# Optimization experiments

Hardware: AMD Instinct MI355X
Metric: run time of the kernel (lower is better)

Reference implementation:

```python
import jax, jax.numpy as jnp
import numpy as np

POOL_H, POOL_W = 7, 7
SCALE = 0.25
SAMPLING = 2  # fixed sampling ratio (static grid)


def _sample_coords(lo, bin_sz, pool, s):
    # lo: [N], bin_sz: [N] -> coords [N, pool*s]
    # point iy within bin: (iy + 0.5) / s of a bin
    offs = (jnp.arange(pool)[:, None] + (jnp.arange(s)[None, :] + 0.5) / s).reshape(-1)  # [pool*s]
    return lo[:, None] + offs[None, :] * bin_sz[:, None]


def roi_align(feat, rois, roibatches):
    B, C, H, W = feat.shape
    N = rois.shape[0]
    x1 = rois[:, 0] * SCALE
    y1 = rois[:, 1] * SCALE
    x2 = rois[:, 2] * SCALE
    y2 = rois[:, 3] * SCALE
    roi_w = jnp.maximum(x2 - x1, 1.0)
    roi_h = jnp.maximum(y2 - y1, 1.0)
    bin_w = roi_w / POOL_W
    bin_h = roi_h / POOL_H

    ys = _sample_coords(y1, bin_h, POOL_H, SAMPLING)  # [N, Gy]
    xs = _sample_coords(x1, bin_w, POOL_W, SAMPLING)  # [N, Gx]
    Gy, Gx = ys.shape[1], xs.shape[1]

    vy = (ys >= -1.0) & (ys <= H)  # out-of-range samples contribute 0
    vx = (xs >= -1.0) & (xs <= W)

    yc = jnp.clip(ys, 0.0, H - 1)
    xc = jnp.clip(xs, 0.0, W - 1)
    y_lo = jnp.clip(jnp.floor(yc).astype(jnp.int32), 0, H - 1)
    x_lo = jnp.clip(jnp.floor(xc).astype(jnp.int32), 0, W - 1)
    y_hi = jnp.minimum(y_lo + 1, H - 1)
    x_hi = jnp.minimum(x_lo + 1, W - 1)
    ly = yc - y_lo  # [N, Gy]
    lx = xc - x_lo  # [N, Gx]
    hy = 1.0 - ly
    hx = 1.0 - lx

    b = roibatches.astype(jnp.int32)[:, None, None]  # [N,1,1]

    def gather(yi, xi):
        # advanced indexing -> [N, Gy, Gx, C]
        return feat[b, :, yi[:, :, None], xi[:, None, :]]

    v_ll = gather(y_lo, x_lo)
    v_lh = gather(y_lo, x_hi)
    v_hl = gather(y_hi, x_lo)
    v_hh = gather(y_hi, x_hi)

    wy_l = (hy * vy)[:, :, None, None]
    wy_h = (ly * vy)[:, :, None, None]
    wx_l = (hx * vx)[:, None, :, None]
    wx_h = (lx * vx)[:, None, :, None]

    vals = (wy_l * wx_l * v_ll + wy_l * wx_h * v_lh
            + wy_h * wx_l * v_hl + wy_h * wx_h * v_hh)  # [N, Gy, Gx, C]

    # average pool over the SAMPLING x SAMPLING points per bin
    vals = vals.reshape(N, POOL_H, SAMPLING, POOL_W, SAMPLING, C)
    out = vals.mean(axis=(2, 4))  # [N, POOL_H, POOL_W, C]
    return jnp.transpose(out, (0, 3, 1, 2))  # [N, C, POOL_H, POOL_W]


def setup_inputs() -> dict:
    key = jax.random.key(0)
    k1, k2, k3, k4 = jax.random.split(key, 4)
    B, C, H, W = 4, 256, 200, 304
    N = 1024
    img_h, img_w = H / SCALE, W / SCALE
    feat = jax.random.normal(k1, (B, C, H, W), dtype=jnp.float32)
    xa = jax.random.uniform(k2, (N, 2), minval=0.0, maxval=img_w)
    ya = jax.random.uniform(k3, (N, 2), minval=0.0, maxval=img_h)
    rois = jnp.stack([xa.min(1), ya.min(1), xa.max(1), ya.max(1)], axis=1).astype(jnp.float32)
    roibatches = jax.random.randint(k4, (N,), 0, B, dtype=jnp.int32)
    return {"feat": feat, "rois": rois, "roibatches": roibatches}


def reference(feat, rois, roibatches):
    return roi_align(feat, rois, roibatches)
```

## Files before the change

### kernel.cpp

```cpp
#include <hip/hip_runtime.h>
#include <hip/hip_bf16.h>


#define POOL 7
constexpr int Bc = 4;
constexpr int Cc = 256;
constexpr int Hc = 200;
constexpr int Wc = 304;
constexpr int HWc = Hc * Wc;
constexpr float SCALEc = 0.25f;
constexpr int STR = 129;

static __device__ __forceinline__ float bf16_lo(unsigned u) {
    u <<= 16;
    return __builtin_bit_cast(float, u);
}
static __device__ __forceinline__ float bf16_hi(unsigned u) {
    u &= 0xFFFF0000u;
    return __builtin_bit_cast(float, u);
}
static __device__ __forceinline__ unsigned pack_bf16(float f0, float f1) {
    unsigned u0 = (unsigned)__hip_bfloat16_raw(__float2bfloat16(f0)).x;
    unsigned u1 = (unsigned)__hip_bfloat16_raw(__float2bfloat16(f1)).x;
    return u0 | (u1 << 16);
}

__global__ __launch_bounds__(1024) void sort_rois_by_batch(
    const int* __restrict__ rb, int* __restrict__ perm, int N)
{
    __shared__ int wave_cnt[16][4];
    __shared__ int bucket_base[4];
    int t    = threadIdx.x;
    int w    = t >> 6;
    int lane = t & 63;
    int b    = (t < N) ? rb[t] : -1;

    unsigned long long m[4];
#pragma unroll
    for (int k = 0; k < 4; ++k) m[k] = __ballot(b == k);
    if (lane == 0) {
#pragma unroll
        for (int k = 0; k < 4; ++k) wave_cnt[w][k] = __popcll(m[k]);
    }
    __syncthreads();
    if (t == 0) {
        int base = 0;
#pragma unroll
        for (int k = 0; k < 4; ++k) {
            int tot = 0;
            for (int ww = 0; ww < 16; ++ww) tot += wave_cnt[ww][k];
            bucket_base[k] = base;
            base += tot;
        }
    }
    __syncthreads();
    if (b >= 0) {
        int rank = bucket_base[b];
        for (int ww = 0; ww < w; ++ww) rank += wave_cnt[ww][b];
        unsigned long long lt = (lane == 0) ? 0ULL : (~0ULL >> (64 - lane));
        rank += __popcll(m[b] & lt);
        perm[rank] = t;
    }
}

__global__ __launch_bounds__(256) void nchw_to_nhwc_bf16(
    const float* __restrict__ in, ushort* __restrict__ outp)
{
    __shared__ float tile[128][65];
    int b  = blockIdx.z;
    int p0 = blockIdx.x * 64;
    int c0 = blockIdx.y * 128;
    int tx = threadIdx.x;
    int ty = threadIdx.y;

    const float* src = in + ((size_t)b * Cc + c0) * (size_t)HWc + p0;
#pragma unroll
    for (int k = 0; k < 32; ++k) {
        int c = ty + 4 * k;
        tile[c][tx ^ ((c >> 5) & 3)] = src[(size_t)c * HWc + tx];
    }
    __syncthreads();

    int t  = ty * 64 + tx;
    int cg = t & 15;
    int pi = t >> 4;
#pragma unroll
    for (int k = 0; k < 4; ++k) {
        int p = pi + 16 * k;
        unsigned u[4];
#pragma unroll
        for (int j = 0; j < 4; ++j) {
            int ce = cg * 8 + 2 * j;
            int co = ce + 1;
            float f0 = tile[ce][p ^ ((ce >> 5) & 3)];
            float f1 = tile[co][p ^ ((co >> 5) & 3)];
            u[j] = pack_bf16(f0, f1);
        }
        size_t d = ((size_t)b * HWc + p0 + p) * (size_t)Cc + c0 + cg * 8;
        *(uint4*)(outp + d) = make_uint4(u[0], u[1], u[2], u[3]);
    }
}

__global__ __launch_bounds__(512, 8) void roialign_gather(
    const ushort* __restrict__ f,
    const float*  __restrict__ rois,
    const int*    __restrict__ rb,
    const int*    __restrict__ perm,
    float*        __restrict__ out)
{
    __shared__ unsigned stage[49 * STR];

    int n    = perm[blockIdx.x];
    int t    = threadIdx.x;
    int wav  = t >> 6;
    int lane = t & 63;

    float x1 = rois[n * 4 + 0] * SCALEc;
    float y1 = rois[n * 4 + 1] * SCALEc;
    float x2 = rois[n * 4 + 2] * SCALEc;
    float y2 = rois[n * 4 + 3] * SCALEc;
    int   b  = rb[n];

    float roi_w = fmaxf(x2 - x1, 1.0f);
    float roi_h = fmaxf(y2 - y1, 1.0f);
    float bin_w = roi_w * (1.0f / POOL);
    float bin_h = roi_h * (1.0f / POOL);

    const uint2* fb = (const uint2*)(f + (size_t)b * ((size_t)HWc * Cc));

#pragma unroll 1
    for (int it = 0; it < 7; ++it) {
        int bin = it * 8 + wav;
        if (bin < 49) {
            int ph = (bin * 9363) >> 16;
            int pw = bin - ph * 7;

            unsigned yrow[2][2];  float wy[2][2];
#pragma unroll
            for (int iy = 0; iy < 2; ++iy) {
                float y  = y1 + ((float)ph + ((float)iy + 0.5f) * 0.5f) * bin_h;
                bool  vy = (y >= -1.0f) && (y <= (float)Hc);
                float yc = fminf(fmaxf(y, 0.0f), (float)(Hc - 1));
                int   y_lo = (int)floorf(yc);
                int   y_hi = min(y_lo + 1, Hc - 1);
                float ly = yc - (float)y_lo;
                yrow[iy][0] = (unsigned)(y_lo * Wc);
                yrow[iy][1] = (unsigned)(y_hi * Wc);
                wy[iy][0] = vy ? (1.0f - ly) : 0.0f;
                wy[iy][1] = vy ? ly : 0.0f;
            }
            unsigned xo[2][2];  float wx[2][2];
#pragma unroll
            for (int ix = 0; ix < 2; ++ix) {
                float x  = x1 + ((float)pw + ((float)ix + 0.5f) * 0.5f) * bin_w;
                bool  vx = (x >= -1.0f) && (x <= (float)Wc);
                float xc = fminf(fmaxf(x, 0.0f), (float)(Wc - 1));
                int   x_lo = (int)floorf(xc);
                int   x_hi = min(x_lo + 1, Wc - 1);
                float lx = xc - (float)x_lo;
                xo[ix][0] = (unsigned)x_lo;
                xo[ix][1] = (unsigned)x_hi;
                wx[ix][0] = vx ? (1.0f - lx) : 0.0f;
                wx[ix][1] = vx ? lx : 0.0f;
            }

            float acc0 = 0.f, acc1 = 0.f, acc2 = 0.f, acc3 = 0.f;
#pragma unroll
            for (int iy = 0; iy < 2; ++iy) {
                uint2 v[8];
#pragma unroll
                for (int q = 0; q < 8; ++q) {
                    int yl = q >> 2, ix = (q >> 1) & 1, xl = q & 1;
                    unsigned p = yrow[iy][yl] + xo[ix][xl];
                    v[q] = fb[(size_t)(p * 64u + (unsigned)lane)];
                }
#pragma unroll
                for (int q = 0; q < 8; ++q) {
                    int yl = q >> 2, ix = (q >> 1) & 1, xl = q & 1;
                    float w = wy[iy][yl] * wx[ix][xl];
                    acc0 = fmaf(w, bf16_lo(v[q].x), acc0);
                    acc1 = fmaf(w, bf16_hi(v[q].x), acc1);
                    acc2 = fmaf(w, bf16_lo(v[q].y), acc2);
                    acc3 = fmaf(w, bf16_hi(v[q].y), acc3);
                }
            }
            unsigned w0 = pack_bf16(acc0 * 0.25f, acc1 * 0.25f);
            unsigned w1 = pack_bf16(acc2 * 0.25f, acc3 * 0.25f);
            *(uint2*)&stage[bin * STR + lane * 2] = make_uint2(w0, w1);
        }
    }
    __syncthreads();

    float* obase = out + (size_t)n * (Cc * POOL * POOL);
#pragma unroll 1
    for (int k = 0; k < 25; ++k) {
        int flat = t + 512 * k;
        if (flat < Cc * POOL * POOL) {
            unsigned c   = ((unsigned)flat * 42800u) >> 21;
            unsigned bin = (unsigned)flat - c * 49u;
            unsigned u   = stage[bin * STR + (c >> 1)];
            obase[flat]  = (c & 1) ? bf16_hi(u) : bf16_lo(u);
        }
    }
}

__global__ __launch_bounds__(256) void roialign_fwd(
    const float* __restrict__ feat,
    const float* __restrict__ rois,
    const int* __restrict__ roibatches,
    float* __restrict__ out,
    int total)
{
    int tid = blockIdx.x * blockDim.x + threadIdx.x;
    if (tid >= total) return;
    int n   = tid / (Cc * POOL * POOL);
    int rem = tid % (Cc * POOL * POOL);
    int c   = rem / (POOL * POOL);
    int bin = rem % (POOL * POOL);
    int ph  = bin / POOL;
    int pw  = bin % POOL;

    float x1 = rois[n * 4 + 0] * SCALEc;
    float y1 = rois[n * 4 + 1] * SCALEc;
    float x2 = rois[n * 4 + 2] * SCALEc;
    float y2 = rois[n * 4 + 3] * SCALEc;
    int   b  = roibatches[n];

    float roi_w = fmaxf(x2 - x1, 1.0f);
    float roi_h = fmaxf(y2 - y1, 1.0f);
    float bin_w = roi_w * (1.0f / POOL);
    float bin_h = roi_h * (1.0f / POOL);

    const float* fp = feat + (size_t)(b * Cc + c) * (size_t)HWc;

    float acc = 0.0f;
#pragma unroll
    for (int iy = 0; iy < 2; ++iy) {
        float y  = y1 + ((float)ph + ((float)iy + 0.5f) * 0.5f) * bin_h;
        bool  vy = (y >= -1.0f) && (y <= (float)Hc);
        float yc = fminf(fmaxf(y, 0.0f), (float)(Hc - 1));
        int   y_lo = (int)floorf(yc);
        int   y_hi = min(y_lo + 1, Hc - 1);
        float ly = yc - (float)y_lo;
        float hy = 1.0f - ly;
        float wyl = vy ? hy : 0.0f;
        float wyh = vy ? ly : 0.0f;
        const float* row_lo = fp + (size_t)y_lo * Wc;
        const float* row_hi = fp + (size_t)y_hi * Wc;
#pragma unroll
        for (int ix = 0; ix < 2; ++ix) {
            float x  = x1 + ((float)pw + ((float)ix + 0.5f) * 0.5f) * bin_w;
            bool  vx = (x >= -1.0f) && (x <= (float)Wc);
            float xc = fminf(fmaxf(x, 0.0f), (float)(Wc - 1));
            int   x_lo = (int)floorf(xc);
            int   x_hi = min(x_lo + 1, Wc - 1);
            float lx = xc - (float)x_lo;
            float hx = 1.0f - lx;
            float wxl = vx ? hx : 0.0f;
            float wxh = vx ? lx : 0.0f;
            acc += wyl * (wxl * row_lo[x_lo] + wxh * row_lo[x_hi])
                 + wyh * (wxl * row_hi[x_lo] + wxh * row_hi[x_hi]);
        }
    }
    out[tid] = acc * 0.25f;
}

extern "C" void kernel_launch(void* const* d_in, const int* in_sizes, int n_in,
                              void* d_out, int out_size, void* d_ws, size_t ws_size,
                              hipStream_t stream)
{
    const float* feat       = (const float*)d_in[0];
    const float* rois       = (const float*)d_in[1];
    const int*   roibatches = (const int*)d_in[2];
    float*       out        = (float*)d_out;
    int N = in_sizes[1] / 4;

    size_t need_nhwc = (size_t)Bc * HWc * Cc * sizeof(ushort);
    size_t need = need_nhwc + (size_t)N * sizeof(int);
    if (ws_size >= need && N <= 1024) {
        ushort* fbh  = (ushort*)d_ws;
        int*    perm = (int*)((char*)d_ws + need_nhwc);

        sort_rois_by_batch<<<1, 1024, 0, stream>>>(roibatches, perm, N);

        dim3 tgrid(HWc / 64, Cc / 128, Bc);
        dim3 tblock(64, 4);
        nchw_to_nhwc_bf16<<<tgrid, tblock, 0, stream>>>(feat, fbh);

        roialign_gather<<<N, 512, 0, stream>>>(fbh, rois, roibatches, perm, out);
    } else {
        int total = out_size;
        roialign_fwd<<<(total + 255) / 256, 256, 0, stream>>>(
            feat, rois, roibatches, out, total);
    }
}
```

Baseline: 128.2 us.

## Load adjacent pixel pairs with 16-byte loads, sort ROIs by y-band, swizzle blocks

The gather kernel now has each half-wave load one of two horizontally adjacent pixels as a uint4 of 8 bf16 channels. This halves the number of load instructions per sample, and the two halves are combined with a cross-lane shuffle. The ROI sort key gains a vertical-center bucket within each batch, and block IDs are interleaved across 8 groups. Both are meant to improve L2 locality and spread concurrent blocks across XCDs. The staging stride is changed to keep uint4 stores aligned. The cost is a longer sort loop, extra shuffles, and some duplicated weight computation.

```diff
diff --git a/kernel.cpp b/kernel.cpp
--- a/kernel.cpp
+++ b/kernel.cpp
@@ -9,7 +9,7 @@
 constexpr int Wc = 304;
 constexpr int HWc = Hc * Wc;
 constexpr float SCALEc = 0.25f;
-constexpr int STR = 129;
+constexpr int STR = 132;
 
 static __device__ __forceinline__ float bf16_lo(unsigned u) {
     u <<= 16;
@@ -25,28 +25,35 @@
     return u0 | (u1 << 16);
 }
 
-__global__ __launch_bounds__(1024) void sort_rois_by_batch(
-    const int* __restrict__ rb, int* __restrict__ perm, int N)
-{
-    __shared__ int wave_cnt[16][4];
-    __shared__ int bucket_base[4];
+__global__ __launch_bounds__(1024) void sort_rois(
+    const float* __restrict__ rois, const int* __restrict__ rb,
+    int* __restrict__ perm, int N)
+{
+    __shared__ int wave_cnt[16][32];
+    __shared__ int bucket_base[32];
     int t    = threadIdx.x;
     int w    = t >> 6;
     int lane = t & 63;
-    int b    = (t < N) ? rb[t] : -1;
-
-    unsigned long long m[4];
-#pragma unroll
-    for (int k = 0; k < 4; ++k) m[k] = __ballot(b == k);
-    if (lane == 0) {
-#pragma unroll
-        for (int k = 0; k < 4; ++k) wave_cnt[w][k] = __popcll(m[k]);
+
+    int key = -1;
+    if (t < N) {
+        int b = rb[t];
+        float yc = (rois[t * 4 + 1] + rois[t * 4 + 3]) * 0.5f * SCALEc;
+        int bucket = min(max((int)(yc * (8.0f / 200.0f)), 0), 7);
+        key = b * 8 + bucket;
+    }
+    unsigned long long lt = (lane == 0) ? 0ULL : (~0ULL >> (64 - lane));
+    int rank_in_wave = 0;
+#pragma unroll 1
+    for (int k = 0; k < 32; ++k) {
+        unsigned long long m = __ballot(key == k);
+        if (lane == 0) wave_cnt[w][k] = __popcll(m);
+        if (key == k)  rank_in_wave = __popcll(m & lt);
     }
     __syncthreads();
     if (t == 0) {
         int base = 0;
-#pragma unroll
-        for (int k = 0; k < 4; ++k) {
+        for (int k = 0; k < 32; ++k) {
             int tot = 0;
             for (int ww = 0; ww < 16; ++ww) tot += wave_cnt[ww][k];
             bucket_base[k] = base;
@@ -54,11 +61,9 @@
         }
     }
     __syncthreads();
-    if (b >= 0) {
-        int rank = bucket_base[b];
-        for (int ww = 0; ww < w; ++ww) rank += wave_cnt[ww][b];
-        unsigned long long lt = (lane == 0) ? 0ULL : (~0ULL >> (64 - lane));
-        rank += __popcll(m[b] & lt);
+    if (key >= 0) {
+        int rank = bucket_base[key] + rank_in_wave;
+        for (int ww = 0; ww < w; ++ww) rank += wave_cnt[ww][key];
         perm[rank] = t;
     }
 }
@@ -110,10 +115,18 @@
 {
     __shared__ unsigned stage[49 * STR];
 
-    int n    = perm[blockIdx.x];
+    int bid = blockIdx.x;
+    int r   = bid;
+    if ((gridDim.x & 7) == 0) {
+        int per = gridDim.x >> 3;
+        r = (bid & 7) * per + (bid >> 3);
+    }
+    int n    = perm[r];
     int t    = threadIdx.x;
     int wav  = t >> 6;
     int lane = t & 63;
+    int half = lane >> 5;
+    int sub  = lane & 31;
 
     float x1 = rois[n * 4 + 0] * SCALEc;
     float y1 = rois[n * 4 + 1] * SCALEc;
@@ -126,7 +139,7 @@
     float bin_w = roi_w * (1.0f / POOL);
     float bin_h = roi_h * (1.0f / POOL);
 
-    const uint2* fb = (const uint2*)(f + (size_t)b * ((size_t)HWc * Cc));
+    const uint4* fb4 = (const uint4*)(f + (size_t)b * ((size_t)HWc * Cc));
 
 #pragma unroll 1
     for (int it = 0; it < 7; ++it) {
@@ -149,7 +162,7 @@
                 wy[iy][0] = vy ? (1.0f - ly) : 0.0f;
                 wy[iy][1] = vy ? ly : 0.0f;
             }
-            unsigned xo[2][2];  float wx[2][2];
+            unsigned xb[2];  float wxh[2];
 #pragma unroll
             for (int ix = 0; ix < 2; ++ix) {
                 float x  = x1 + ((float)pw + ((float)ix + 0.5f) * 0.5f) * bin_w;
@@ -158,35 +171,51 @@
                 int   x_lo = (int)floorf(xc);
                 int   x_hi = min(x_lo + 1, Wc - 1);
                 float lx = xc - (float)x_lo;
-                xo[ix][0] = (unsigned)x_lo;
-                xo[ix][1] = (unsigned)x_hi;
-                wx[ix][0] = vx ? (1.0f - lx) : 0.0f;
-                wx[ix][1] = vx ? lx : 0.0f;
+                float wx0 = vx ? (1.0f - lx) : 0.0f;
+                float wx1 = vx ? lx : 0.0f;
+                int   bx  = min(x_lo, Wc - 2);
+                int   off_lo = x_lo - bx;
+                int   off_hi = x_hi - bx;
+                float w0 = (off_lo == 0 ? wx0 : 0.0f) + (off_hi == 0 ? wx1 : 0.0f);
+                float w1 = (off_lo == 1 ? wx0 : 0.0f) + (off_hi == 1 ? wx1 : 0.0f);
+                xb[ix]  = (unsigned)bx;
+                wxh[ix] = half ? w1 : w0;
             }
 
-            float acc0 = 0.f, acc1 = 0.f, acc2 = 0.f, acc3 = 0.f;
+            float acc[8] = {0.f, 0.f, 0.f, 0.f, 0.f, 0.f, 0.f, 0.f};
 #pragma unroll
             for (int iy = 0; iy < 2; ++iy) {
-                uint2 v[8];
-#pragma unroll
-                for (int q = 0; q < 8; ++q) {
-                    int yl = q >> 2, ix = (q >> 1) & 1, xl = q & 1;
-                    unsigned p = yrow[iy][yl] + xo[ix][xl];
-                    v[q] = fb[(size_t)(p * 64u + (unsigned)lane)];
+                uint4 v[4];
+#pragma unroll
+                for (int q = 0; q < 4; ++q) {
+                    int yl = q >> 1, ix = q & 1;
+                    unsigned pix = yrow[iy][yl] + xb[ix];
+                    v[q] = fb4[(size_t)(pix * 32u + (unsigned)lane)];
                 }
 #pragma unroll
-                for (int q = 0; q < 8; ++q) {
-                    int yl = q >> 2, ix = (q >> 1) & 1, xl = q & 1;
-                    float w = wy[iy][yl] * wx[ix][xl];
-                    acc0 = fmaf(w, bf16_lo(v[q].x), acc0);
-                    acc1 = fmaf(w, bf16_hi(v[q].x), acc1);
-                    acc2 = fmaf(w, bf16_lo(v[q].y), acc2);
-                    acc3 = fmaf(w, bf16_hi(v[q].y), acc3);
+                for (int q = 0; q < 4; ++q) {
+                    int yl = q >> 1, ix = q & 1;
+                    float w = wy[iy][yl] * wxh[ix];
+                    acc[0] = fmaf(w, bf16_lo(v[q].x), acc[0]);
+                    acc[1] = fmaf(w, bf16_hi(v[q].x), acc[1]);
+                    acc[2] = fmaf(w, bf16_lo(v[q].y), acc[2]);
+                    acc[3] = fmaf(w, bf16_hi(v[q].y), acc[3]);
+                    acc[4] = fmaf(w, bf16_lo(v[q].z), acc[4]);
+                    acc[5] = fmaf(w, bf16_hi(v[q].z), acc[5]);
+                    acc[6] = fmaf(w, bf16_lo(v[q].w), acc[6]);
+                    acc[7] = fmaf(w, bf16_hi(v[q].w), acc[7]);
                 }
             }
-            unsigned w0 = pack_bf16(acc0 * 0.25f, acc1 * 0.25f);
-            unsigned w1 = pack_bf16(acc2 * 0.25f, acc3 * 0.25f);
-            *(uint2*)&stage[bin * STR + lane * 2] = make_uint2(w0, w1);
+#pragma unroll
+            for (int j = 0; j < 8; ++j) acc[j] += __shfl_xor(acc[j], 32);
+
+            if (half == 0) {
+                unsigned p0 = pack_bf16(acc[0] * 0.25f, acc[1] * 0.25f);
+                unsigned p1 = pack_bf16(acc[2] * 0.25f, acc[3] * 0.25f);
+                unsigned p2 = pack_bf16(acc[4] * 0.25f, acc[5] * 0.25f);
+                unsigned p3 = pack_bf16(acc[6] * 0.25f, acc[7] * 0.25f);
+                *(uint4*)&stage[bin * STR + sub * 4] = make_uint4(p0, p1, p2, p3);
+            }
         }
     }
     __syncthreads();
@@ -281,7 +310,7 @@
         ushort* fbh  = (ushort*)d_ws;
         int*    perm = (int*)((char*)d_ws + need_nhwc);
 
-        sort_rois_by_batch<<<1, 1024, 0, stream>>>(roibatches, perm, N);
+        sort_rois<<<1, 1024, 0, stream>>>(rois, roibatches, perm, N);
 
         dim3 tgrid(HWc / 64, Cc / 128, Bc);
         dim3 tblock(64, 4);
```

Result: slower. 134.9 us (+5.2%).

## Split channels into 32-wide groups with blocked bf16 layout and per-group ROI blocks

Applied to the files above, without the earlier changes.

Changes the bf16 workspace layout from NHWC to [B][C/32][H][W][32] channel-group blocks and launches eight blocks per ROI, each handling one 32-channel group across all 49 bins at once. Each wave covers 8 bins with 8 lanes per bin, so a pixel's 64-byte channel chunk stays contiguous and the working set per block is a smaller plane slice. The aim is better cache locality per group and more parallelism, with fp32 staging replacing the packed bf16 stage. In exchange, per-ROI coordinate math runs eight times and each gather is a narrower 64-byte access.

```diff
diff --git a/kernel.cpp b/kernel.cpp
--- a/kernel.cpp
+++ b/kernel.cpp
@@ -9,7 +9,6 @@
 constexpr int Wc = 304;
 constexpr int HWc = Hc * Wc;
 constexpr float SCALEc = 0.25f;
-constexpr int STR = 129;
 
 static __device__ __forceinline__ float bf16_lo(unsigned u) {
     u <<= 16;
@@ -63,7 +62,7 @@
     }
 }
 
-__global__ __launch_bounds__(256) void nchw_to_nhwc_bf16(
+__global__ __launch_bounds__(256) void nchw_to_cg32_bf16(
     const float* __restrict__ in, ushort* __restrict__ outp)
 {
     __shared__ float tile[128][65];
@@ -81,39 +80,45 @@
     }
     __syncthreads();
 
-    int t  = ty * 64 + tx;
-    int cg = t & 15;
-    int pi = t >> 4;
-#pragma unroll
-    for (int k = 0; k < 4; ++k) {
-        int p = pi + 16 * k;
+    int t   = ty * 64 + tx;
+    int ch8 = (t & 3) * 8;
+    int p   = t >> 2;
+#pragma unroll
+    for (int cgl = 0; cgl < 4; ++cgl) {
+        int cg = (c0 >> 5) + cgl;
         unsigned u[4];
 #pragma unroll
         for (int j = 0; j < 4; ++j) {
-            int ce = cg * 8 + 2 * j;
+            int ce = cgl * 32 + ch8 + 2 * j;
             int co = ce + 1;
             float f0 = tile[ce][p ^ ((ce >> 5) & 3)];
             float f1 = tile[co][p ^ ((co >> 5) & 3)];
             u[j] = pack_bf16(f0, f1);
         }
-        size_t d = ((size_t)b * HWc + p0 + p) * (size_t)Cc + c0 + cg * 8;
+        size_t d = ((size_t)(b * 8 + cg) * HWc + p0 + p) * 32 + ch8;
         *(uint4*)(outp + d) = make_uint4(u[0], u[1], u[2], u[3]);
     }
 }
 
-__global__ __launch_bounds__(512, 8) void roialign_gather(
+__global__ __launch_bounds__(512, 8) void roialign_gather_cg(
     const ushort* __restrict__ f,
     const float*  __restrict__ rois,
     const int*    __restrict__ rb,
     const int*    __restrict__ perm,
     float*        __restrict__ out)
 {
-    __shared__ unsigned stage[49 * STR];
-
-    int n    = perm[blockIdx.x];
+    __shared__ float stage[32 * 50];
+
+    int bid  = blockIdx.x;
+    int cg   = bid & 7;
+    int r    = bid >> 3;
+    int n    = perm[r];
     int t    = threadIdx.x;
-    int wav  = t >> 6;
+    int w    = t >> 6;
     int lane = t & 63;
+    int oct  = lane >> 3;
+    int cs   = lane & 7;
+    int bin  = w * 8 + oct;
 
     float x1 = rois[n * 4 + 0] * SCALEc;
     float y1 = rois[n * 4 + 1] * SCALEc;
@@ -126,80 +131,77 @@
     float bin_w = roi_w * (1.0f / POOL);
     float bin_h = roi_h * (1.0f / POOL);
 
-    const uint2* fb = (const uint2*)(f + (size_t)b * ((size_t)HWc * Cc));
-
-#pragma unroll 1
-    for (int it = 0; it < 7; ++it) {
-        int bin = it * 8 + wav;
-        if (bin < 49) {
-            int ph = (bin * 9363) >> 16;
-            int pw = bin - ph * 7;
-
-            unsigned yrow[2][2];  float wy[2][2];
-#pragma unroll
-            for (int iy = 0; iy < 2; ++iy) {
-                float y  = y1 + ((float)ph + ((float)iy + 0.5f) * 0.5f) * bin_h;
-                bool  vy = (y >= -1.0f) && (y <= (float)Hc);
-                float yc = fminf(fmaxf(y, 0.0f), (float)(Hc - 1));
-                int   y_lo = (int)floorf(yc);
-                int   y_hi = min(y_lo + 1, Hc - 1);
-                float ly = yc - (float)y_lo;
-                yrow[iy][0] = (unsigned)(y_lo * Wc);
-                yrow[iy][1] = (unsigned)(y_hi * Wc);
-                wy[iy][0] = vy ? (1.0f - ly) : 0.0f;
-                wy[iy][1] = vy ? ly : 0.0f;
+    const uint2* fb = (const uint2*)(f + (size_t)(b * 8 + cg) * ((size_t)HWc * 32));
+
+    if (bin < 49) {
+        int ph = (bin * 9363) >> 16;
+        int pw = bin - ph * 7;
+
+        unsigned yrow[2][2];  float wy[2][2];
+#pragma unroll
+        for (int iy = 0; iy < 2; ++iy) {
+            float y  = y1 + ((float)ph + ((float)iy + 0.5f) * 0.5f) * bin_h;
+            bool  vy = (y >= -1.0f) && (y <= (float)Hc);
+            float yc = fminf(fmaxf(y, 0.0f), (float)(Hc - 1));
+            int   y_lo = (int)floorf(yc);
+            int   y_hi = min(y_lo + 1, Hc - 1);
+            float ly = yc - (float)y_lo;
+            yrow[iy][0] = (unsigned)(y_lo * Wc);
+            yrow[iy][1] = (unsigned)(y_hi * Wc);
+            wy[iy][0] = vy ? (1.0f - ly) : 0.0f;
+            wy[iy][1] = vy ? ly : 0.0f;
+        }
+        unsigned xo[2][2];  float wx[2][2];
+#pragma unroll
+        for (int ix = 0; ix < 2; ++ix) {
+            float x  = x1 + ((float)pw + ((float)ix + 0.5f) * 0.5f) * bin_w;
+            bool  vx = (x >= -1.0f) && (x <= (float)Wc);
+            float xc = fminf(fmaxf(x, 0.0f), (float)(Wc - 1));
+            int   x_lo = (int)floorf(xc);
+            int   x_hi = min(x_lo + 1, Wc - 1);
+            float lx = xc - (float)x_lo;
+            xo[ix][0] = (unsigned)x_lo;
+            xo[ix][1] = (unsigned)x_hi;
+            wx[ix][0] = vx ? (1.0f - lx) : 0.0f;
+            wx[ix][1] = vx ? lx : 0.0f;
+        }
+
+        float acc0 = 0.f, acc1 = 0.f, acc2 = 0.f, acc3 = 0.f;
+#pragma unroll
+        for (int iy = 0; iy < 2; ++iy) {
+            uint2 v[8];
+#pragma unroll
+            for (int q = 0; q < 8; ++q) {
+                int yl = q >> 2, ix = (q >> 1) & 1, xl = q & 1;
+                unsigned pix = yrow[iy][yl] + xo[ix][xl];
+                v[q] = fb[(size_t)pix * 8u + (unsigned)cs];
             }
-            unsigned xo[2][2];  float wx[2][2];
-#pragma unroll
-            for (int ix = 0; ix < 2; ++ix) {
-                float x  = x1 + ((float)pw + ((float)ix + 0.5f) * 0.5f) * bin_w;
-                bool  vx = (x >= -1.0f) && (x <= (float)Wc);
-                float xc = fminf(fmaxf(x, 0.0f), (float)(Wc - 1));
-                int   x_lo = (int)floorf(xc);
-                int   x_hi = min(x_lo + 1, Wc - 1);
-                float lx = xc - (float)x_lo;
-                xo[ix][0] = (unsigned)x_lo;
-                xo[ix][1] = (unsigned)x_hi;
-                wx[ix][0] = vx ? (1.0f - lx) : 0.0f;
-                wx[ix][1] = vx ? lx : 0.0f;
+#pragma unroll
+            for (int q = 0; q < 8; ++q) {
+                int yl = q >> 2, ix = (q >> 1) & 1, xl = q & 1;
+                float wq = wy[iy][yl] * wx[ix][xl];
+                acc0 = fmaf(wq, bf16_lo(v[q].x), acc0);
+                acc1 = fmaf(wq, bf16_hi(v[q].x), acc1);
+                acc2 = fmaf(wq, bf16_lo(v[q].y), acc2);
+                acc3 = fmaf(wq, bf16_hi(v[q].y), acc3);
             }
-
-            float acc0 = 0.f, acc1 = 0.f, acc2 = 0.f, acc3 = 0.f;
-#pragma unroll
-            for (int iy = 0; iy < 2; ++iy) {
-                uint2 v[8];
-#pragma unroll
-                for (int q = 0; q < 8; ++q) {
-                    int yl = q >> 2, ix = (q >> 1) & 1, xl = q & 1;
-                    unsigned p = yrow[iy][yl] + xo[ix][xl];
-                    v[q] = fb[(size_t)(p * 64u + (unsigned)lane)];
-                }
-#pragma unroll
-                for (int q = 0; q < 8; ++q) {
-                    int yl = q >> 2, ix = (q >> 1) & 1, xl = q & 1;
-                    float w = wy[iy][yl] * wx[ix][xl];
-                    acc0 = fmaf(w, bf16_lo(v[q].x), acc0);
-                    acc1 = fmaf(w, bf16_hi(v[q].x), acc1);
-                    acc2 = fmaf(w, bf16_lo(v[q].y), acc2);
-                    acc3 = fmaf(w, bf16_hi(v[q].y), acc3);
-                }
-            }
-            unsigned w0 = pack_bf16(acc0 * 0.25f, acc1 * 0.25f);
-            unsigned w1 = pack_bf16(acc2 * 0.25f, acc3 * 0.25f);
-            *(uint2*)&stage[bin * STR + lane * 2] = make_uint2(w0, w1);
-        }
-    }
-    __syncthreads();
-
-    float* obase = out + (size_t)n * (Cc * POOL * POOL);
-#pragma unroll 1
-    for (int k = 0; k < 25; ++k) {
+        }
+        int ch = cs * 4;
+        stage[(ch + 0) * 50 + bin] = acc0 * 0.25f;
+        stage[(ch + 1) * 50 + bin] = acc1 * 0.25f;
+        stage[(ch + 2) * 50 + bin] = acc2 * 0.25f;
+        stage[(ch + 3) * 50 + bin] = acc3 * 0.25f;
+    }
+    __syncthreads();
+
+    float* obase = out + (size_t)n * (Cc * POOL * POOL) + (size_t)cg * (32 * POOL * POOL);
+#pragma unroll
+    for (int k = 0; k < 4; ++k) {
         int flat = t + 512 * k;
-        if (flat < Cc * POOL * POOL) {
-            unsigned c   = ((unsigned)flat * 42800u) >> 21;
-            unsigned bin = (unsigned)flat - c * 49u;
-            unsigned u   = stage[bin * STR + (c >> 1)];
-            obase[flat]  = (c & 1) ? bf16_hi(u) : bf16_lo(u);
+        if (flat < 32 * POOL * POOL) {
+            unsigned c    = ((unsigned)flat * 42800u) >> 21;
+            unsigned bn   = (unsigned)flat - c * 49u;
+            obase[flat] = stage[c * 50 + bn];
         }
     }
 }
@@ -275,19 +277,19 @@
     float*       out        = (float*)d_out;
     int N = in_sizes[1] / 4;
 
-    size_t need_nhwc = (size_t)Bc * HWc * Cc * sizeof(ushort);
-    size_t need = need_nhwc + (size_t)N * sizeof(int);
+    size_t need_copy = (size_t)Bc * HWc * Cc * sizeof(ushort);
+    size_t need = need_copy + (size_t)N * sizeof(int);
     if (ws_size >= need && N <= 1024) {
         ushort* fbh  = (ushort*)d_ws;
-        int*    perm = (int*)((char*)d_ws + need_nhwc);
+        int*    perm = (int*)((char*)d_ws + need_copy);
 
         sort_rois_by_batch<<<1, 1024, 0, stream>>>(roibatches, perm, N);
 
         dim3 tgrid(HWc / 64, Cc / 128, Bc);
         dim3 tblock(64, 4);
-        nchw_to_nhwc_bf16<<<tgrid, tblock, 0, stream>>>(feat, fbh);
-
-        roialign_gather<<<N, 512, 0, stream>>>(fbh, rois, roibatches, perm, out);
+        nchw_to_cg32_bf16<<<tgrid, tblock, 0, stream>>>(feat, fbh);
+
+        roialign_gather_cg<<<N * 8, 512, 0, stream>>>(fbh, rois, roibatches, perm, out);
     } else {
         int total = out_size;
         roialign_fwd<<<(total + 255) / 256, 256, 0, stream>>>(
```

Result: faster. 121.9 us, median of 2 (-4.9%).
